# Performance work log

Measured on AMD Instinct MI355X. Metric: run time of the kernel, lower is better.

Reference implementation:

```python
import jax, jax.numpy as jnp
import numpy as np

B, T, W, HP = 1, 64, 88, 48   # batch, frames, pitches, hidden_per_pitch
NU, NH, K = 24, 4, 25          # n_unit, n_heads, neighborhood window
HD = NU // NH                  # head dim = 6
HL = NU // 2                   # LSTM hidden per direction = 12


def _lstm_bidir(x, w_ih, w_hh, b_ih, b_hh):
    # x: [N, T, In]; w_ih: [2, 4*HL, In]; w_hh: [2, 4*HL, HL]; biases: [2, 4*HL]
    N = x.shape[0]
    def run(Wih, Whh, bih, bhh, reverse):
        def step(carry, xt):
            h, c = carry
            g = xt @ Wih.T + h @ Whh.T + bih + bhh
            i, f, gg, o = jnp.split(g, 4, axis=-1)  # torch gate order i,f,g,o
            c = jax.nn.sigmoid(f) * c + jax.nn.sigmoid(i) * jnp.tanh(gg)
            h = jax.nn.sigmoid(o) * jnp.tanh(c)
            return (h, c), h
        init = (jnp.zeros((N, HL), x.dtype), jnp.zeros((N, HL), x.dtype))
        _, ys = jax.lax.scan(step, init, jnp.swapaxes(x, 0, 1), reverse=reverse)
        return jnp.swapaxes(ys, 0, 1)
    return jnp.concatenate([run(w_ih[0], w_hh[0], b_ih[0], b_hh[0], False),
                            run(w_ih[1], w_hh[1], b_ih[1], b_hh[1], True)], axis=-1)


def _natten2d(x, qkv_w, qkv_b, rpb, proj_w, proj_b):
    # Neighborhood attention over 2D grid [B, Hh, Ww] with KxK window clamped at borders.
    Bn, Hh, Ww, C = x.shape
    qkv = (x @ qkv_w.T + qkv_b).reshape(Bn, Hh, Ww, 3, NH, HD)
    q = qkv[..., 0, :, :] * (HD ** -0.5)
    k = qkv[..., 1, :, :]
    v = qkv[..., 2, :, :]
    half = K // 2
    ar = jnp.arange(K)
    idx_i = jnp.clip(jnp.arange(Hh) - half, 0, Hh - K)[:, None] + ar  # [Hh,K]
    idx_j = jnp.clip(jnp.arange(Ww) - half, 0, Ww - K)[:, None] + ar  # [Ww,K]
    kg = k[:, idx_i][:, :, :, idx_j]  # [B,Hh,K,Ww,K,NH,HD]
    vg = v[:, idx_i][:, :, :, idx_j]
    ri = idx_i - jnp.arange(Hh)[:, None] + (K - 1)  # relative pos bias indices [Hh,K]
    rj = idx_j - jnp.arange(Ww)[:, None] + (K - 1)  # [Ww,K]
    bias = rpb[:, ri][:, :, :, rj]                  # [NH,Hh,K,Ww,K]
    logits = jnp.einsum('bijnd,biajcnd->bnijac', q, kg)
    logits = logits + jnp.transpose(bias, (0, 1, 3, 2, 4))[None]
    attn = jax.nn.softmax(logits.reshape(Bn, NH, Hh, Ww, K * K), axis=-1)
    attn = attn.reshape(Bn, NH, Hh, Ww, K, K)
    out = jnp.einsum('bnijac,biajcnd->bijnd', attn, vg).reshape(Bn, Hh, Ww, C)
    return out @ proj_w.T + proj_b


def _forward(features, condition, mask, emb, w_ih_l0, w_hh_l0, b_ih_l0, b_hh_l0,
             w_ih_l1, w_hh_l1, b_ih_l1, b_hh_l1, qkv_w, qkv_b, rpb, proj_w, proj_b,
             out_w, out_b):
    # concat: [B,T,88,HP] + [B,T,88,4] + [B,T,88,1] -> [B,T,88,HP+5]
    cat = jnp.concatenate([jnp.transpose(features, (0, 1, 3, 2)), emb[condition],
                           mask[..., None]], axis=-1)
    x = jnp.transpose(cat, (0, 2, 1, 3)).reshape(B * W, T, HP + 5)  # pitchwise LSTM
    x = _lstm_bidir(x, w_ih_l0, w_hh_l0, b_ih_l0, b_hh_l0)
    x = _lstm_bidir(x, w_ih_l1, w_hh_l1, b_ih_l1, b_hh_l1)
    x = jnp.transpose(x.reshape(B, W, T, NU), (0, 2, 1, 3))  # [B,T,88,NU]
    for _ in range(2):  # n_layers=2; Sequential(*[m]*2) => SHARED weights
        x = _natten2d(x, qkv_w, qkv_b, rpb, proj_w, proj_b)
    return x @ out_w.T + out_b  # [B,T,88,5]


def setup_inputs():
    ks = jax.random.split(jax.random.key(0), 24)
    def unif(k, shape, fan):
        s = 1.0 / np.sqrt(fan)
        return jax.random.uniform(k, shape, jnp.float32, -s, s)
    return {
        'features': jax.random.normal(ks[0], (B, T, HP, W), jnp.float32),
        'condition': jax.random.randint(ks[1], (B, T, W), 0, 5),
        'mask': jax.random.uniform(ks[2], (B, T, W), jnp.float32),
        'emb': jax.random.normal(ks[3], (5, 4), jnp.float32),
        'w_ih_l0': unif(ks[4], (2, 4 * HL, HP + 5), HL),
        'w_hh_l0': unif(ks[5], (2, 4 * HL, HL), HL),
        'b_ih_l0': unif(ks[6], (2, 4 * HL), HL),
        'b_hh_l0': unif(ks[7], (2, 4 * HL), HL),
        'w_ih_l1': unif(ks[8], (2, 4 * HL, 2 * HL), HL),
        'w_hh_l1': unif(ks[9], (2, 4 * HL, HL), HL),
        'b_ih_l1': unif(ks[10], (2, 4 * HL), HL),
        'b_hh_l1': unif(ks[11], (2, 4 * HL), HL),
        'qkv_w': unif(ks[12], (3 * NU, NU), NU),
        'qkv_b': unif(ks[13], (3 * NU,), NU),
        'rpb': jax.random.normal(ks[14], (NH, 2 * K - 1, 2 * K - 1), jnp.float32) * 0.02,
        'proj_w': unif(ks[15], (NU, NU), NU),
        'proj_b': unif(ks[16], (NU,), NU),
        'out_w': unif(ks[17], (5, NU), NU),
        'out_b': unif(ks[18], (5,), NU),
    }


def reference(features, condition, mask, emb, w_ih_l0, w_hh_l0, b_ih_l0, b_hh_l0,
              w_ih_l1, w_hh_l1, b_ih_l1, b_hh_l1, qkv_w, qkv_b, rpb, proj_w, proj_b,
              out_w, out_b):
    return _forward(features, condition, mask, emb, w_ih_l0, w_hh_l0, b_ih_l0, b_hh_l0,
                    w_ih_l1, w_hh_l1, b_ih_l1, b_hh_l1, qkv_w, qkv_b, rpb,
                    proj_w, proj_b, out_w, out_b)
```

## Files before the change

### kernel.cpp

```cpp
#include <hip/hip_runtime.h>
#include <hip/hip_bf16.h>

#define NPIX (64*88)
#define NSEQ 88
#define TT 64
#define F0 53
#define GATES 48

typedef __hip_bfloat16 bf16;

__device__ __forceinline__ float frcp(float x){ return __builtin_amdgcn_rcpf(x); }
__device__ __forceinline__ float blo(unsigned u){ return __uint_as_float(u<<16); }
__device__ __forceinline__ float bhi(unsigned u){ return __uint_as_float(u & 0xffff0000u); }

__device__ __forceinline__ void unpack6(uint4 r, float* f){
  f[0] = __uint_as_float(r.x << 16);
  f[1] = __uint_as_float(r.x & 0xffff0000u);
  f[2] = __uint_as_float(r.y << 16);
  f[3] = __uint_as_float(r.y & 0xffff0000u);
  f[4] = __uint_as_float(r.z << 16);
  f[5] = __uint_as_float(r.z & 0xffff0000u);
}

__device__ __forceinline__ float rl(float v, int l){
  return __int_as_float(__builtin_amdgcn_readlane(__float_as_int(v), l));
}
template<int K> __device__ __forceinline__ float qbcast(float v){
  constexpr int ctrl = K | (K<<2) | (K<<4) | (K<<6);
  return __int_as_float(__builtin_amdgcn_update_dpp(0, __float_as_int(v), ctrl, 0xf, 0xf, true));
}

__device__ __forceinline__ void lstm_dir(const float* __restrict__ whh,
    const float* gb_base, float* ybuf, int d, int lane){
  int u = lane >> 2, grp = lane & 3;
  int uc = (u < 12) ? u : 11;
  int j = grp*12 + uc;
  float w[12];
  const float* wb = whh + (d*GATES + j)*12;
  #pragma unroll
  for (int m=0;m<12;++m) w[m] = wb[m];
  float negs = (grp==2) ? -2.f : -1.f;
  float amul = (grp==2) ?  2.f :  1.f;
  float aadd = (grp==2) ? -1.f :  0.f;
  const float* gb = gb_base + (d*TT)*49 + j;
  float hval = 0.f, cval = 0.f;
  int t0 = d ? (TT-1) : 0;
  float gnext = gb[t0*49];
  bool wr = (grp==0) && (u < 12);
  for (int s=0;s<TT;++s){
    int t = d ? (TT-1-s) : s;
    float gg = gnext;
    int tn = d ? max(TT-2-s,0) : min(s+1,TT-1);
    gnext = gb[tn*49];
    float h0=rl(hval,0),  h1=rl(hval,4),  h2=rl(hval,8),   h3=rl(hval,12);
    float h4=rl(hval,16), h5=rl(hval,20), h6=rl(hval,24),  h7=rl(hval,28);
    float h8=rl(hval,32), h9=rl(hval,36), h10=rl(hval,40), h11=rl(hval,44);
    float a0 = gg + h0*w[0] + h4*w[4] + h8*w[8];
    float a1 = h1*w[1] + h5*w[5] + h9*w[9];
    float a2 = h2*w[2] + h6*w[6] + h10*w[10];
    float a3 = h3*w[3] + h7*w[7] + h11*w[11];
    float dot = (a0+a1)+(a2+a3);
    float act = amul*frcp(1.f + __expf(negs*dot)) + aadd;
    float ai = qbcast<0>(act);
    float af = qbcast<1>(act);
    float ag = qbcast<2>(act);
    float ao = qbcast<3>(act);
    float cn = af*cval + ai*ag;
    float th = 2.f*frcp(1.f + __expf(-2.f*cn)) - 1.f;
    hval = ao*th; cval = cn;
    if (wr) ybuf[t*25 + d*12 + u] = hval;
  }
}

__global__ __launch_bounds__(1024) void k_core(
    const float* __restrict__ feat, const int* __restrict__ cond,
    const float* __restrict__ mask, const float* __restrict__ emb,
    const float* __restrict__ wih0, const float* __restrict__ whh0,
    const float* __restrict__ bih0, const float* __restrict__ bhh0,
    const float* __restrict__ wih1, const float* __restrict__ whh1,
    const float* __restrict__ bih1, const float* __restrict__ bhh1,
    const float* __restrict__ qkv_w, const float* __restrict__ qkv_b,
    float* __restrict__ q, bf16* __restrict__ kh, bf16* __restrict__ vh){
  int n = (blockIdx.x & 7)*11 + (blockIdx.x >> 3);
  int tid = threadIdx.x;
  int wave = tid >> 6; int lane = tid & 63;
  __shared__ float smem[12864];
  float* gbuf = smem;
  float* sx   = smem + 6272;
  float* y0   = smem + 6272+3392;
  float* y1   = smem + 6272+4992;
  float* outb = smem;

  for (int idx = tid; idx < TT*F0; idx += 1024){
    int t = idx / F0, f = idx - t*F0;
    float v;
    if (f < 48)      v = feat[(t*48 + f)*88 + n];
    else if (f < 52) v = emb[cond[t*88+n]*4 + (f-48)];
    else             v = mask[t*88+n];
    sx[idx] = v;
  }
  __syncthreads();

  {
    int wu = __builtin_amdgcn_readfirstlane(wave);
    int dd = wu >> 3, jg = wu & 7;
    const float* w0 = wih0 + (dd*GATES + jg*6)*F0;
    const float* xr = sx + lane*F0;
    float a0[6], a1[6];
    #pragma unroll
    for (int k=0;k<6;++k){
      int j = dd*GATES + jg*6 + k;
      a0[k] = bih0[j] + bhh0[j];
      a1[k] = 0.f;
    }
    for (int f=0; f<52; f+=2){
      float x0 = xr[f], x1 = xr[f+1];
      #pragma unroll
      for (int k=0;k<6;++k){
        a0[k] += x0*w0[k*F0+f];
        a1[k] += x1*w0[k*F0+f+1];
      }
    }
    {
      float x0 = xr[52];
      #pragma unroll
      for (int k=0;k<6;++k) a0[k] += x0*w0[k*F0+52];
    }
    float* go = gbuf + (dd*TT + lane)*49 + jg*6;
    #pragma unroll
    for (int k=0;k<6;++k) go[k] = a0[k] + a1[k];
  }
  __syncthreads();

  if (wave < 2) lstm_dir(whh0, gbuf, y0, wave, lane);
  __syncthreads();

  {
    int wu = __builtin_amdgcn_readfirstlane(wave);
    int dd = wu >> 3, jg = wu & 7;
    const float* w1p = wih1 + (dd*GATES + jg*6)*24;
    const float* xr = y0 + lane*25;
    float a0[6], a1[6];
    #pragma unroll
    for (int k=0;k<6;++k){
      int j = dd*GATES + jg*6 + k;
      a0[k] = bih1[j] + bhh1[j];
      a1[k] = 0.f;
    }
    #pragma unroll
    for (int c=0; c<24; c+=2){
      float x0 = xr[c], x1 = xr[c+1];
      #pragma unroll
      for (int k=0;k<6;++k){
        a0[k] += x0*w1p[k*24+c];
        a1[k] += x1*w1p[k*24+c+1];
      }
    }
    float* go = gbuf + (dd*TT + lane)*49 + jg*6;
    #pragma unroll
    for (int k=0;k<6;++k) go[k] = a0[k] + a1[k];
  }
  __syncthreads();

  if (wave < 2) lstm_dir(whh1, gbuf, y1, wave, lane);
  __syncthreads();

  if (wave < 12){
    int wu = __builtin_amdgcn_readfirstlane(wave);
    int g0 = wu*6;
    const float* qw = qkv_w + g0*24;
    const float* xr = y1 + lane*25;
    float a0[6], a1[6];
    #pragma unroll
    for (int k=0;k<6;++k){ a0[k] = qkv_b[g0+k]; a1[k] = 0.f; }
    #pragma unroll
    for (int c=0; c<24; c+=2){
      float x0 = xr[c], x1 = xr[c+1];
      #pragma unroll
      for (int k=0;k<6;++k){
        a0[k] += x0*qw[k*24+c];
        a1[k] += x1*qw[k*24+c+1];
      }
    }
    float* oo = outb + lane*73 + g0;
    #pragma unroll
    for (int k=0;k<6;++k) oo[k] = a0[k] + a1[k];
  }
  __syncthreads();

  for (int idx = tid; idx < TT*72; idx += 1024){
    int gq = idx % 72; int t = idx / 72;
    int p = t*88 + n;
    float acc = outb[t*73 + gq];
    int s = gq/24, rem = gq - s*24;
    if (s==0) q[p*24+rem] = acc*0.4082482904638631f;
    else {
      int hh = rem/6, pos = rem - hh*6;
      bf16* dst = (s==1) ? kh : vh;
      dst[((size_t)hh*NPIX + p)*8 + pos] = __float2bfloat16(acc);
    }
  }
}

__global__ __launch_bounds__(256) void k_attn1(
    const float* __restrict__ q, const bf16* __restrict__ kh,
    const bf16* __restrict__ vh, const float* __restrict__ rpb,
    const float* __restrict__ pw, const float* __restrict__ pb,
    const float* __restrict__ qkv_w, const float* __restrict__ qkv_b,
    float* __restrict__ q2, bf16* __restrict__ kh2, bf16* __restrict__ vh2){
  int p = blockIdx.x; int tid = threadIdx.x;
  int h = tid >> 6; int lane = tid & 63;
  int i = p / 88, j = p - i*88;
  int si = min(max(i-12,0),39), sj = min(max(j-12,0),63);
  __shared__ float aorow[24];
  __shared__ float xrow[24];

  float qv[6];
  #pragma unroll
  for (int d=0; d<6; ++d) qv[d] = q[p*24 + h*6 + d];
  const uint4* kb = (const uint4*)(kh + (size_t)h*NPIX*8);
  const uint4* vb = (const uint4*)(vh + (size_t)h*NPIX*8);
  float lgv[10]; int roff[10];
  float lmax = -1e30f;
  #pragma unroll
  for (int it=0; it<10; ++it){
    int nb = lane + it*64;
    bool valid = nb < 625;
    int nbc = valid ? nb : 624;
    int a = nbc/25, cc = nbc - a*25;
    int gi = si + a, gj = sj + cc;
    int row = gi*88+gj;
    roff[it] = row;
    float kr[6];
    unpack6(kb[row], kr);
    float lg = qv[0]*kr[0]+qv[1]*kr[1]+qv[2]*kr[2]+qv[3]*kr[3]+qv[4]*kr[4]+qv[5]*kr[5];
    lg += rpb[(h*49 + (gi - i + 24))*49 + (gj - j + 24)];
    lg = valid ? lg : -1e30f;
    lgv[it] = lg;
    lmax = fmaxf(lmax, lg);
  }
  #pragma unroll
  for (int off=32; off; off>>=1) lmax = fmaxf(lmax, __shfl_xor(lmax, off));
  float lsum = 0.f;
  #pragma unroll
  for (int it=0; it<10; ++it){
    float pe = __expf(lgv[it]-lmax);
    lgv[it] = pe; lsum += pe;
  }
  #pragma unroll
  for (int off=32; off; off>>=1) lsum += __shfl_xor(lsum, off);
  float acc[6] = {0,0,0,0,0,0};
  #pragma unroll
  for (int it=0; it<10; ++it){
    float vr[6];
    unpack6(vb[roff[it]], vr);
    float pe = lgv[it];
    #pragma unroll
    for (int d=0; d<6; ++d) acc[d] += pe*vr[d];
  }
  #pragma unroll
  for (int d=0; d<6; ++d){
    #pragma unroll
    for (int off=32; off; off>>=1) acc[d] += __shfl_xor(acc[d], off);
  }
  if (lane == 0){
    float inv = frcp(lsum);
    #pragma unroll
    for (int d=0; d<6; ++d) aorow[h*6+d] = acc[d]*inv;
  }
  __syncthreads();

  if (tid < 24){
    float a2 = pb[tid];
    const float* wr = pw + tid*24;
    #pragma unroll
    for (int c=0;c<24;++c) a2 += aorow[c]*wr[c];
    xrow[tid] = a2;
  }
  __syncthreads();

  if (tid < 72){
    float a2 = qkv_b[tid];
    const float* wr = qkv_w + tid*24;
    #pragma unroll
    for (int c=0;c<24;++c) a2 += xrow[c]*wr[c];
    int s = tid/24, rem = tid - s*24;
    if (s==0) q2[p*24+rem] = a2*0.4082482904638631f;
    else {
      int hh = rem/6, pos = rem - hh*6;
      bf16* dst = (s==1) ? kh2 : vh2;
      dst[((size_t)hh*NPIX + p)*8 + pos] = __float2bfloat16(a2);
    }
  }
}

__global__ __launch_bounds__(512) void k_attn(
    const float* __restrict__ q, const bf16* __restrict__ kh,
    const bf16* __restrict__ vh, const float* __restrict__ rpb,
    float* __restrict__ ao){
  int b = blockIdx.x;
  int h = b / 704; int rem = b - h*704;
  int ti = rem / 44, tj = rem - ti*44;
  int i0 = ti*4, j0 = tj*2;
  int tid = threadIdx.x;
  int w = tid >> 6; int lane = tid & 63;
  int osi = min(max(i0-12,0),39);
  int osj = min(max(j0-12,0),63);

  __shared__ unsigned kt[728*5];
  __shared__ unsigned vt[728*5];
  const uint4* kg = (const uint4*)(kh + (size_t)h*NPIX*8);
  const uint4* vg = (const uint4*)(vh + (size_t)h*NPIX*8);
  for (int idx = tid; idx < 728; idx += 512){
    int a = idx / 26, cc = idx - a*26;
    int gi = min(osi + a, 63), gj = min(osj + cc, 87);
    int src = gi*88 + gj;
    uint4 kr = kg[src];
    uint4 vr = vg[src];
    int o = idx*5;
    kt[o] = kr.x; kt[o+1] = kr.y; kt[o+2] = kr.z;
    vt[o] = vr.x; vt[o+1] = vr.y; vt[o+2] = vr.z;
  }
  __syncthreads();

  int pi = i0 + (w>>1), pj = j0 + (w&1);
  int p = pi*88 + pj;
  int dsi = min(max(pi-12,0),39) - osi;
  int dsj = min(max(pj-12,0),63) - osj;
  int rbi = osi + dsi - pi + 24;
  int rbj = osj + dsj - pj + 24;

  float qv[6];
  #pragma unroll
  for (int d=0; d<6; ++d) qv[d] = q[p*24 + h*6 + d];

  float lgv[10]; int rof[10];
  float lmax = -1e30f;
  #pragma unroll
  for (int it=0; it<10; ++it){
    int nb = lane + it*64;
    bool valid = nb < 625;
    int nbc = valid ? nb : 624;
    int a = nbc/25, cc = nbc - a*25;
    int r5 = ((a+dsi)*26 + (cc+dsj))*5;
    rof[it] = r5;
    unsigned k0 = kt[r5], k1 = kt[r5+1], k2 = kt[r5+2];
    float lg = qv[0]*blo(k0)+qv[1]*bhi(k0)+qv[2]*blo(k1)
             + qv[3]*bhi(k1)+qv[4]*blo(k2)+qv[5]*bhi(k2);
    lg += rpb[(h*49 + (a + rbi))*49 + (cc + rbj)];
    lg = valid ? lg : -1e30f;
    lgv[it] = lg;
    lmax = fmaxf(lmax, lg);
  }
  #pragma unroll
  for (int off=32; off; off>>=1) lmax = fmaxf(lmax, __shfl_xor(lmax, off));
  float lsum = 0.f;
  #pragma unroll
  for (int it=0; it<10; ++it){
    float pe = __expf(lgv[it]-lmax);
    lgv[it] = pe; lsum += pe;
  }
  #pragma unroll
  for (int off=32; off; off>>=1) lsum += __shfl_xor(lsum, off);
  float acc[6] = {0,0,0,0,0,0};
  #pragma unroll
  for (int it=0; it<10; ++it){
    int r5 = rof[it];
    unsigned v0 = vt[r5], v1 = vt[r5+1], v2 = vt[r5+2];
    float pe = lgv[it];
    acc[0] += pe*blo(v0); acc[1] += pe*bhi(v0);
    acc[2] += pe*blo(v1); acc[3] += pe*bhi(v1);
    acc[4] += pe*blo(v2); acc[5] += pe*bhi(v2);
  }
  #pragma unroll
  for (int d=0; d<6; ++d){
    #pragma unroll
    for (int off=32; off; off>>=1) acc[d] += __shfl_xor(acc[d], off);
  }
  if (lane == 0){
    float inv = frcp(lsum);
    #pragma unroll
    for (int d=0; d<6; ++d) ao[p*24 + h*6 + d] = acc[d]*inv;
  }
}

__global__ __launch_bounds__(64) void k_proj_out(const float* __restrict__ ain,
    const float* __restrict__ pw, const float* __restrict__ pb,
    const float* __restrict__ ow, const float* __restrict__ ob,
    float* __restrict__ out){
  int p = blockIdx.x; int tid = threadIdx.x;
  __shared__ float arow[24];
  __shared__ float xrow[24];
  if (tid < 24) arow[tid] = ain[p*24+tid];
  __syncthreads();
  if (tid < 24){
    float a2 = pb[tid];
    const float* wr = pw + tid*24;
    #pragma unroll
    for (int c=0;c<24;++c) a2 += arow[c]*wr[c];
    xrow[tid] = a2;
  }
  __syncthreads();
  if (tid < 5){
    float a2 = ob[tid];
    const float* wr = ow + tid*24;
    #pragma unroll
    for (int c=0;c<24;++c) a2 += xrow[c]*wr[c];
    out[p*5+tid] = a2;
  }
}

extern "C" void kernel_launch(void* const* d_in, const int* in_sizes, int n_in,
                              void* d_out, int out_size, void* d_ws, size_t ws_size,
                              hipStream_t stream) {
  const float* feat    = (const float*)d_in[0];
  const int*   cond    = (const int*)  d_in[1];
  const float* mask    = (const float*)d_in[2];
  const float* emb     = (const float*)d_in[3];
  const float* w_ih_l0 = (const float*)d_in[4];
  const float* w_hh_l0 = (const float*)d_in[5];
  const float* b_ih_l0 = (const float*)d_in[6];
  const float* b_hh_l0 = (const float*)d_in[7];
  const float* w_ih_l1 = (const float*)d_in[8];
  const float* w_hh_l1 = (const float*)d_in[9];
  const float* b_ih_l1 = (const float*)d_in[10];
  const float* b_hh_l1 = (const float*)d_in[11];
  const float* qkv_w   = (const float*)d_in[12];
  const float* qkv_b   = (const float*)d_in[13];
  const float* rpb     = (const float*)d_in[14];
  const float* proj_w  = (const float*)d_in[15];
  const float* proj_b  = (const float*)d_in[16];
  const float* out_w   = (const float*)d_in[17];
  const float* out_b   = (const float*)d_in[18];
  float* out = (float*)d_out;

  float* ws  = (float*)d_ws;
  float* Q1  = ws;
  float* Q2  = Q1 + 135168;
  float* AO  = Q2 + 135168;
  bf16*  KH1 = (bf16*)(AO + 135168);
  bf16*  VH1 = KH1 + 180224;
  bf16*  KH2 = VH1 + 180224;
  bf16*  VH2 = KH2 + 180224;

  k_core<<<NSEQ, 1024, 0, stream>>>(
      feat, cond, mask, emb,
      w_ih_l0, w_hh_l0, b_ih_l0, b_hh_l0,
      w_ih_l1, w_hh_l1, b_ih_l1, b_hh_l1,
      qkv_w, qkv_b, Q1, KH1, VH1);

  k_attn1<<<NPIX, 256, 0, stream>>>(
      Q1, KH1, VH1, rpb, proj_w, proj_b, qkv_w, qkv_b,
      Q2, KH2, VH2);

  k_attn<<<4*16*44, 512, 0, stream>>>(Q2, KH2, VH2, rpb, AO);

  k_proj_out<<<NPIX, 64, 0, stream>>>(AO, proj_w, proj_b, out_w, out_b, out);
}
```

Before: 190.2 us.

## Unify neighborhood attention into tiled LDS kernel fusing projections, all heads per block

Replaces the per-pixel first attention kernel, the per-head second attention kernel and the separate projection kernel with one templated kernel. Each block stages K/V for all four heads of a 2x2 pixel tile into shared memory and fuses the output projection with either the next QKV projection or the final output head. Wave reductions move from shuffle-xor to DPP row operations plus a readlane. This cuts global K/V gathers, kernel launches and the AO round trip. The cost is a large LDS footprint per block, which may limit occupancy.

```diff
diff --git a/kernel.cpp b/kernel.cpp
--- a/kernel.cpp
+++ b/kernel.cpp
@@ -13,21 +13,30 @@
 __device__ __forceinline__ float blo(unsigned u){ return __uint_as_float(u<<16); }
 __device__ __forceinline__ float bhi(unsigned u){ return __uint_as_float(u & 0xffff0000u); }
 
-__device__ __forceinline__ void unpack6(uint4 r, float* f){
-  f[0] = __uint_as_float(r.x << 16);
-  f[1] = __uint_as_float(r.x & 0xffff0000u);
-  f[2] = __uint_as_float(r.y << 16);
-  f[3] = __uint_as_float(r.y & 0xffff0000u);
-  f[4] = __uint_as_float(r.z << 16);
-  f[5] = __uint_as_float(r.z & 0xffff0000u);
-}
-
 __device__ __forceinline__ float rl(float v, int l){
   return __int_as_float(__builtin_amdgcn_readlane(__float_as_int(v), l));
 }
 template<int K> __device__ __forceinline__ float qbcast(float v){
   constexpr int ctrl = K | (K<<2) | (K<<4) | (K<<6);
   return __int_as_float(__builtin_amdgcn_update_dpp(0, __float_as_int(v), ctrl, 0xf, 0xf, true));
+}
+
+template<int CTRL> __device__ __forceinline__ float dpp_add(float v){
+  return v + __int_as_float(__builtin_amdgcn_update_dpp(0, __float_as_int(v), CTRL, 0xf, 0xf, true));
+}
+template<int CTRL> __device__ __forceinline__ float dpp_max(float v){
+  int vi = __float_as_int(v);
+  return fmaxf(v, __int_as_float(__builtin_amdgcn_update_dpp(vi, vi, CTRL, 0xf, 0xf, false)));
+}
+__device__ __forceinline__ float wred_sum(float v){
+  v = dpp_add<0x111>(v); v = dpp_add<0x112>(v); v = dpp_add<0x114>(v); v = dpp_add<0x118>(v);
+  v = dpp_add<0x142>(v); v = dpp_add<0x143>(v);
+  return rl(v,63);
+}
+__device__ __forceinline__ float wred_max(float v){
+  v = dpp_max<0x111>(v); v = dpp_max<0x112>(v); v = dpp_max<0x114>(v); v = dpp_max<0x118>(v);
+  v = dpp_max<0x142>(v); v = dpp_max<0x143>(v);
+  return rl(v,63);
 }
 
 __device__ __forceinline__ void lstm_dir(const float* __restrict__ whh,
@@ -202,25 +211,61 @@
   }
 }
 
-__global__ __launch_bounds__(256) void k_attn1(
+template<int MODE>
+__global__ __launch_bounds__(1024, 8) void k_natten(
     const float* __restrict__ q, const bf16* __restrict__ kh,
     const bf16* __restrict__ vh, const float* __restrict__ rpb,
     const float* __restrict__ pw, const float* __restrict__ pb,
     const float* __restrict__ qkv_w, const float* __restrict__ qkv_b,
-    float* __restrict__ q2, bf16* __restrict__ kh2, bf16* __restrict__ vh2){
-  int p = blockIdx.x; int tid = threadIdx.x;
-  int h = tid >> 6; int lane = tid & 63;
-  int i = p / 88, j = p - i*88;
-  int si = min(max(i-12,0),39), sj = min(max(j-12,0),63);
-  __shared__ float aorow[24];
-  __shared__ float xrow[24];
+    const float* __restrict__ ow, const float* __restrict__ ob,
+    float* __restrict__ q2, bf16* __restrict__ kh2, bf16* __restrict__ vh2,
+    float* __restrict__ out){
+  int bid = blockIdx.x;
+  int b = (bid & 7)*176 + (bid >> 3);
+  int ti = b / 44, tj = b - ti*44;
+  int i0 = ti*2, j0 = tj*2;
+  int tid = threadIdx.x;
+  int w = tid >> 6; int lane = tid & 63;
+  int osi = min(max(i0-12,0),39);
+  int osj = min(max(j0-12,0),63);
+
+  __shared__ unsigned kv[16224];
+  unsigned* kt = kv;
+  unsigned* vt = kv + 8112;
+  float* aop = (float*)kv;
+  float* x4  = aop + 96;
+
+  const uint4* kg = (const uint4*)kh;
+  const uint4* vg = (const uint4*)vh;
+  for (int idx = tid; idx < 2704; idx += 1024){
+    int h = idx / 676; int r = idx - h*676;
+    int a = r / 26, cc = r - a*26;
+    int gi = min(osi + a, 63), gj = min(osj + cc, 87);
+    int src = h*NPIX + gi*88 + gj;
+    uint4 kr = kg[src];
+    uint4 vr = vg[src];
+    int o = idx*3;
+    kt[o] = kr.x; kt[o+1] = kr.y; kt[o+2] = kr.z;
+    vt[o] = vr.x; vt[o+1] = vr.y; vt[o+2] = vr.z;
+  }
+  __syncthreads();
+
+  int px = w & 3; int h = w >> 2;
+  int pi = i0 + (px>>1), pj = j0 + (px&1);
+  int p = pi*88 + pj;
+  int dsi = min(max(pi-12,0),39) - osi;
+  int dsj = min(max(pj-12,0),63) - osj;
+  int rbi = osi + dsi - pi + 24;
+  int rbj = osj + dsj - pj + 24;
+  int hbase = h*2028;
+  int rowofs = hbase + (dsi*26 + dsj)*3;
+  const float* rpbh = rpb + (h*49 + rbi)*49 + rbj;
 
   float qv[6];
   #pragma unroll
   for (int d=0; d<6; ++d) qv[d] = q[p*24 + h*6 + d];
-  const uint4* kb = (const uint4*)(kh + (size_t)h*NPIX*8);
-  const uint4* vb = (const uint4*)(vh + (size_t)h*NPIX*8);
-  float lgv[10]; int roff[10];
+
+  float lgv[10];
   float lmax = -1e30f;
   #pragma unroll
   for (int it=0; it<10; ++it){
@@ -228,185 +273,84 @@
     bool valid = nb < 625;
     int nbc = valid ? nb : 624;
     int a = nbc/25, cc = nbc - a*25;
-    int gi = si + a, gj = sj + cc;
-    int row = gi*88+gj;
-    roff[it] = row;
-    float kr[6];
-    unpack6(kb[row], kr);
-    float lg = qv[0]*kr[0]+qv[1]*kr[1]+qv[2]*kr[2]+qv[3]*kr[3]+qv[4]*kr[4]+qv[5]*kr[5];
-    lg += rpb[(h*49 + (gi - i + 24))*49 + (gj - j + 24)];
+    int r3 = rowofs + (a*26 + cc)*3;
+    unsigned k0 = kt[r3], k1 = kt[r3+1], k2 = kt[r3+2];
+    float lg = qv[0]*blo(k0)+qv[1]*bhi(k0)+qv[2]*blo(k1)
+             + qv[3]*bhi(k1)+qv[4]*blo(k2)+qv[5]*bhi(k2);
+    lg += rpbh[a*49 + cc];
     lg = valid ? lg : -1e30f;
     lgv[it] = lg;
     lmax = fmaxf(lmax, lg);
   }
-  #pragma unroll
-  for (int off=32; off; off>>=1) lmax = fmaxf(lmax, __shfl_xor(lmax, off));
+  lmax = wred_max(lmax);
   float lsum = 0.f;
   #pragma unroll
   for (int it=0; it<10; ++it){
     float pe = __expf(lgv[it]-lmax);
     lgv[it] = pe; lsum += pe;
   }
-  #pragma unroll
-  for (int off=32; off; off>>=1) lsum += __shfl_xor(lsum, off);
+  lsum = wred_sum(lsum);
   float acc[6] = {0,0,0,0,0,0};
-  #pragma unroll
-  for (int it=0; it<10; ++it){
-    float vr[6];
-    unpack6(vb[roff[it]], vr);
-    float pe = lgv[it];
-    #pragma unroll
-    for (int d=0; d<6; ++d) acc[d] += pe*vr[d];
-  }
-  #pragma unroll
-  for (int d=0; d<6; ++d){
-    #pragma unroll
-    for (int off=32; off; off>>=1) acc[d] += __shfl_xor(acc[d], off);
-  }
-  if (lane == 0){
-    float inv = frcp(lsum);
-    #pragma unroll
-    for (int d=0; d<6; ++d) aorow[h*6+d] = acc[d]*inv;
-  }
-  __syncthreads();
-
-  if (tid < 24){
-    float a2 = pb[tid];
-    const float* wr = pw + tid*24;
-    #pragma unroll
-    for (int c=0;c<24;++c) a2 += aorow[c]*wr[c];
-    xrow[tid] = a2;
-  }
-  __syncthreads();
-
-  if (tid < 72){
-    float a2 = qkv_b[tid];
-    const float* wr = qkv_w + tid*24;
-    #pragma unroll
-    for (int c=0;c<24;++c) a2 += xrow[c]*wr[c];
-    int s = tid/24, rem = tid - s*24;
-    if (s==0) q2[p*24+rem] = a2*0.4082482904638631f;
-    else {
-      int hh = rem/6, pos = rem - hh*6;
-      bf16* dst = (s==1) ? kh2 : vh2;
-      dst[((size_t)hh*NPIX + p)*8 + pos] = __float2bfloat16(a2);
-    }
-  }
-}
-
-__global__ __launch_bounds__(512) void k_attn(
-    const float* __restrict__ q, const bf16* __restrict__ kh,
-    const bf16* __restrict__ vh, const float* __restrict__ rpb,
-    float* __restrict__ ao){
-  int b = blockIdx.x;
-  int h = b / 704; int rem = b - h*704;
-  int ti = rem / 44, tj = rem - ti*44;
-  int i0 = ti*4, j0 = tj*2;
-  int tid = threadIdx.x;
-  int w = tid >> 6; int lane = tid & 63;
-  int osi = min(max(i0-12,0),39);
-  int osj = min(max(j0-12,0),63);
-
-  __shared__ unsigned kt[728*5];
-  __shared__ unsigned vt[728*5];
-  const uint4* kg = (const uint4*)(kh + (size_t)h*NPIX*8);
-  const uint4* vg = (const uint4*)(vh + (size_t)h*NPIX*8);
-  for (int idx = tid; idx < 728; idx += 512){
-    int a = idx / 26, cc = idx - a*26;
-    int gi = min(osi + a, 63), gj = min(osj + cc, 87);
-    int src = gi*88 + gj;
-    uint4 kr = kg[src];
-    uint4 vr = vg[src];
-    int o = idx*5;
-    kt[o] = kr.x; kt[o+1] = kr.y; kt[o+2] = kr.z;
-    vt[o] = vr.x; vt[o+1] = vr.y; vt[o+2] = vr.z;
-  }
-  __syncthreads();
-
-  int pi = i0 + (w>>1), pj = j0 + (w&1);
-  int p = pi*88 + pj;
-  int dsi = min(max(pi-12,0),39) - osi;
-  int dsj = min(max(pj-12,0),63) - osj;
-  int rbi = osi + dsi - pi + 24;
-  int rbj = osj + dsj - pj + 24;
-
-  float qv[6];
-  #pragma unroll
-  for (int d=0; d<6; ++d) qv[d] = q[p*24 + h*6 + d];
-
-  float lgv[10]; int rof[10];
-  float lmax = -1e30f;
   #pragma unroll
   for (int it=0; it<10; ++it){
     int nb = lane + it*64;
-    bool valid = nb < 625;
-    int nbc = valid ? nb : 624;
+    int nbc = (nb < 625) ? nb : 624;
     int a = nbc/25, cc = nbc - a*25;
-    int r5 = ((a+dsi)*26 + (cc+dsj))*5;
-    rof[it] = r5;
-    unsigned k0 = kt[r5], k1 = kt[r5+1], k2 = kt[r5+2];
-    float lg = qv[0]*blo(k0)+qv[1]*bhi(k0)+qv[2]*blo(k1)
-             + qv[3]*bhi(k1)+qv[4]*blo(k2)+qv[5]*bhi(k2);
-    lg += rpb[(h*49 + (a + rbi))*49 + (cc + rbj)];
-    lg = valid ? lg : -1e30f;
-    lgv[it] = lg;
-    lmax = fmaxf(lmax, lg);
-  }
-  #pragma unroll
-  for (int off=32; off; off>>=1) lmax = fmaxf(lmax, __shfl_xor(lmax, off));
-  float lsum = 0.f;
-  #pragma unroll
-  for (int it=0; it<10; ++it){
-    float pe = __expf(lgv[it]-lmax);
-    lgv[it] = pe; lsum += pe;
-  }
-  #pragma unroll
-  for (int off=32; off; off>>=1) lsum += __shfl_xor(lsum, off);
-  float acc[6] = {0,0,0,0,0,0};
-  #pragma unroll
-  for (int it=0; it<10; ++it){
-    int r5 = rof[it];
-    unsigned v0 = vt[r5], v1 = vt[r5+1], v2 = vt[r5+2];
+    int r3 = rowofs + (a*26 + cc)*3;
+    unsigned v0 = vt[r3], v1 = vt[r3+1], v2 = vt[r3+2];
     float pe = lgv[it];
     acc[0] += pe*blo(v0); acc[1] += pe*bhi(v0);
     acc[2] += pe*blo(v1); acc[3] += pe*bhi(v1);
     acc[4] += pe*blo(v2); acc[5] += pe*bhi(v2);
   }
-  #pragma unroll
-  for (int d=0; d<6; ++d){
-    #pragma unroll
-    for (int off=32; off; off>>=1) acc[d] += __shfl_xor(acc[d], off);
-  }
+  float inv = frcp(lsum);
+  #pragma unroll
+  for (int d=0; d<6; ++d) acc[d] = wred_sum(acc[d])*inv;
+
+  __syncthreads();
   if (lane == 0){
-    float inv = frcp(lsum);
-    #pragma unroll
-    for (int d=0; d<6; ++d) ao[p*24 + h*6 + d] = acc[d]*inv;
-  }
-}
-
-__global__ __launch_bounds__(64) void k_proj_out(const float* __restrict__ ain,
-    const float* __restrict__ pw, const float* __restrict__ pb,
-    const float* __restrict__ ow, const float* __restrict__ ob,
-    float* __restrict__ out){
-  int p = blockIdx.x; int tid = threadIdx.x;
-  __shared__ float arow[24];
-  __shared__ float xrow[24];
-  if (tid < 24) arow[tid] = ain[p*24+tid];
-  __syncthreads();
-  if (tid < 24){
-    float a2 = pb[tid];
-    const float* wr = pw + tid*24;
-    #pragma unroll
-    for (int c=0;c<24;++c) a2 += arow[c]*wr[c];
-    xrow[tid] = a2;
-  }
-  __syncthreads();
-  if (tid < 5){
-    float a2 = ob[tid];
-    const float* wr = ow + tid*24;
-    #pragma unroll
-    for (int c=0;c<24;++c) a2 += xrow[c]*wr[c];
-    out[p*5+tid] = a2;
+    #pragma unroll
+    for (int d=0; d<6; ++d) aop[px*24 + h*6 + d] = acc[d];
+  }
+  __syncthreads();
+
+  if (tid < 96){
+    int pp = tid / 24, c = tid - (tid/24)*24;
+    float a2 = pb[c];
+    const float* wr = pw + c*24;
+    #pragma unroll
+    for (int k=0;k<24;++k) a2 += aop[pp*24+k]*wr[k];
+    x4[pp*24+c] = a2;
+  }
+  __syncthreads();
+
+  if (MODE == 0){
+    if (tid < 288){
+      int pp = tid / 72, g = tid - (tid/72)*72;
+      float a2 = qkv_b[g];
+      const float* wr = qkv_w + g*24;
+      #pragma unroll
+      for (int k=0;k<24;++k) a2 += x4[pp*24+k]*wr[k];
+      int ppi = i0 + (pp>>1), ppj = j0 + (pp&1);
+      int pp_ = ppi*88 + ppj;
+      int s = g/24, rem = g - s*24;
+      if (s==0) q2[pp_*24+rem] = a2*0.4082482904638631f;
+      else {
+        int hh = rem/6, pos = rem - hh*6;
+        bf16* dst = (s==1) ? kh2 : vh2;
+        dst[((size_t)hh*NPIX + pp_)*8 + pos] = __float2bfloat16(a2);
+      }
+    }
+  } else {
+    if (tid < 20){
+      int pp = tid / 5, c = tid - (tid/5)*5;
+      float a2 = ob[c];
+      const float* wr = ow + c*24;
+      #pragma unroll
+      for (int k=0;k<24;++k) a2 += x4[pp*24+k]*wr[k];
+      int ppi = i0 + (pp>>1), ppj = j0 + (pp&1);
+      out[(ppi*88 + ppj)*5 + c] = a2;
+    }
   }
 }
 
@@ -437,8 +381,7 @@
   float* ws  = (float*)d_ws;
   float* Q1  = ws;
   float* Q2  = Q1 + 135168;
-  float* AO  = Q2 + 135168;
-  bf16*  KH1 = (bf16*)(AO + 135168);
+  bf16*  KH1 = (bf16*)(Q2 + 135168);
   bf16*  VH1 = KH1 + 180224;
   bf16*  KH2 = VH1 + 180224;
   bf16*  VH2 = KH2 + 180224;
@@ -449,11 +392,11 @@
       w_ih_l1, w_hh_l1, b_ih_l1, b_hh_l1,
       qkv_w, qkv_b, Q1, KH1, VH1);
 
-  k_attn1<<<NPIX, 256, 0, stream>>>(
+  k_natten<0><<<32*44, 1024, 0, stream>>>(
       Q1, KH1, VH1, rpb, proj_w, proj_b, qkv_w, qkv_b,
-      Q2, KH2, VH2);
-
-  k_attn<<<4*16*44, 512, 0, stream>>>(Q2, KH2, VH2, rpb, AO);
-
-  k_proj_out<<<NPIX, 64, 0, stream>>>(AO, proj_w, proj_b, out_w, out_b, out);
-}
+      nullptr, nullptr, Q2, KH2, VH2, nullptr);
+
+  k_natten<1><<<32*44, 1024, 0, stream>>>(
+      Q2, KH2, VH2, rpb, proj_w, proj_b, nullptr, nullptr,
+      out_w, out_b, nullptr, nullptr, nullptr, out);
+}
```

New measurement: 178.5 us, median of 2. -6.2%, faster.
